# Kernel tuning notes

Hardware: AMD Instinct MI355X
Metric: run time of the kernel (lower is better)

## Reference

```python
import jax, jax.numpy as jnp
import numpy as np

SCALE = 16.0
IGNORE_THRESH = 0.5
BAD_CONF_WEIGHT = 1.25
NUM_CLASSES = 4
ANCHORS_PX = np.array([[16,16],[32,32],[64,64],[128,128],[256,256],[32,64],[64,32],[128,64],[64,128]], dtype=np.float32)


def _bce_logits(x, z):
    # stable binary_cross_entropy_with_logits, elementwise
    return jnp.maximum(x, 0.0) - x * z + jnp.log1p(jnp.exp(-jnp.abs(x)))


def _inv_tanh(y):
    mid = 0.5 * jnp.log((1.0 + y) / (1.0 - y))
    return jnp.where(y <= -1.0, -2.0, jnp.where(y >= 1.0, 2.0, mid))


def _iou_cxcywh(box1, box2):
    # matches bbox_iou(x1y1x2y2=False): (cx, cy, half_w, half_h) with +1 area convention
    b1x1, b1x2 = box1[:, 0] - box1[:, 2], box1[:, 0] + box1[:, 2]
    b1y1, b1y2 = box1[:, 1] - box1[:, 3], box1[:, 1] + box1[:, 3]
    b2x1, b2x2 = box2[:, 0] - box2[:, 2], box2[:, 0] + box2[:, 2]
    b2y1, b2y2 = box2[:, 1] - box2[:, 3], box2[:, 1] + box2[:, 3]
    iw = jnp.clip(jnp.minimum(b1x2, b2x2) - jnp.maximum(b1x1, b2x1) + 1.0, 0.0)
    ih = jnp.clip(jnp.minimum(b1y2, b2y2) - jnp.maximum(b1y1, b2y1) + 1.0, 0.0)
    inter = iw * ih
    a1 = (b1x2 - b1x1 + 1.0) * (b1y2 - b1y1 + 1.0)
    a2 = (b2x2 - b2x1 + 1.0) * (b2y2 - b2y1 + 1.0)
    return inter / (a1 + a2 - inter + 1e-16)


def _yolo_loss(prediction, target, target_sizes):
    nB, nA, nH, nW = prediction.shape[:4]
    nC = NUM_CLASSES
    anchors = jnp.asarray(ANCHORS_PX) / SCALE  # grid units, [nA,2]
    x = prediction[..., 1]
    y = prediction[..., 2]
    w = prediction[..., 5]
    h = prediction[..., 4]
    pred_conf = prediction[..., 0]
    pred_cls = prediction[..., 6:]
    grid_x = jnp.arange(nW, dtype=jnp.float32)[None, None, None, :]
    grid_y = jnp.arange(nH, dtype=jnp.float32)[None, None, :, None]
    aw4 = anchors[:, 0][None, :, None, None]
    ah4 = anchors[:, 1][None, :, None, None]
    xd, yd, wd, hd = map(jax.lax.stop_gradient, (x, y, w, h))  # torch uses .data
    pred_boxes = jnp.stack([
        jnp.tanh(xd) + 0.5 + grid_x + 0.0 * yd,
        jnp.tanh(yd) + 0.5 + grid_y + 0.0 * xd,
        jnp.exp(wd) * aw4,
        jnp.exp(hd) * ah4,
    ], axis=-1)  # [nB,nA,nH,nW,4]

    # target[:, :, [0,1,3,4]] /= scale (targets are constants w.r.t. grad)
    col_scale = jnp.ones(target.shape[-1], jnp.float32).at[jnp.array([0, 1, 3, 4])].set(1.0 / SCALE)
    tgt = jax.lax.stop_gradient(target) * col_scale

    pred_conf_sg = jax.lax.stop_gradient(pred_conf)
    pred_cls_sg = jax.lax.stop_gradient(pred_cls)
    b_idx = jnp.arange(nB)
    a_idx = jnp.arange(nA)
    awv = anchors[:, 0]
    ahv = anchors[:, 1]
    anchor_area = (awv + 1.0) * (ahv + 1.0)
    T = tgt.shape[1]
    ts_arr = target_sizes.astype(jnp.int32)
    zeros = jnp.zeros((nB, nA, nH, nW), jnp.float32)
    carry0 = dict(mask=zeros, conf_mask=jnp.ones_like(zeros), tx=zeros, ty=zeros, tw=zeros,
                  th=zeros, tconf=zeros, tcls=jnp.zeros((nB, nA, nH, nW, nC), jnp.float32),
                  nGT=jnp.zeros((), jnp.int32), nCorrect=jnp.zeros((), jnp.int32))

    def step(c, xs):
        t, row = xs  # row: [nB, 13+nC]
        gx, gy, gh_, gw_ = row[:, 0], row[:, 1], row[:, 3], row[:, 4]
        valid = (t < ts_arr) & (gw_ != 0) & (gh_ != 0)
        gi = jnp.clip(gx.astype(jnp.int32), 0, nW - 1)
        gj = jnp.clip(gy.astype(jnp.int32), 0, nH - 1)
        # anchor IoU (boxes [0,0,w,h] as corners, +1 convention) -> [nB,nA]
        inter = (jnp.minimum(gw_[:, None], awv[None, :]) + 1.0) * (jnp.minimum(gh_[:, None], ahv[None, :]) + 1.0)
        anch_ious = inter / ((gw_ + 1.0)[:, None] * (gh_ + 1.0)[:, None] + anchor_area[None, :] - inter + 1e-16)
        ii = (b_idx[:, None], a_idx[None, :], gj[:, None], gi[:, None])
        cm = c['conf_mask']
        cm = cm.at[ii].set(jnp.where(valid[:, None] & (anch_ious > IGNORE_THRESH), 0.0, cm[ii]))
        best_n = jnp.argmax(anch_ious, axis=1)
        idx = (b_idx, best_n, gj, gi)

        def setv(A, val):
            return A.at[idx].set(jnp.where(valid, val, A[idx]))

        mask = setv(c['mask'], 1.0)
        cm = setv(cm, 1.0)
        tx_ = setv(c['tx'], _inv_tanh(gx - (gi.astype(jnp.float32) + 0.5)))
        ty_ = setv(c['ty'], _inv_tanh(gy - (gj.astype(jnp.float32) + 0.5)))
        tw_ = setv(c['tw'], jnp.log(gw_ / awv[best_n] + 1e-16))
        th_ = setv(c['th'], jnp.log(gh_ / ahv[best_n] + 1e-16))
        tconf_ = setv(c['tconf'], 1.0)
        cls_row = row[:, 13:]
        tcls_ = c['tcls'].at[idx].set(jnp.where(valid[:, None], cls_row, c['tcls'][idx]))
        nGT = c['nGT'] + valid.sum().astype(jnp.int32)
        pb = pred_boxes[idx]  # [nB,4]
        iou = _iou_cxcywh(jnp.stack([gx, gy, gw_, gh_], axis=1), pb)
        plabel = jnp.argmax(pred_cls_sg[idx], axis=-1)
        score = pred_conf_sg[idx]
        correct = valid & (iou > 0.5) & (plabel == jnp.argmax(cls_row, axis=-1)) & (score > 0)
        nCorrect = c['nCorrect'] + correct.sum().astype(jnp.int32)
        return dict(mask=mask, conf_mask=cm, tx=tx_, ty=ty_, tw=tw_, th=th_, tconf=tconf_,
                    tcls=tcls_, nGT=nGT, nCorrect=nCorrect), None

    carry, _ = jax.lax.scan(step, carry0, (jnp.arange(T, dtype=jnp.int32), jnp.swapaxes(tgt, 0, 1)))

    mask = carry['mask']
    conf_mask = carry['conf_mask']
    cmf = conf_mask - mask  # conf_mask_false

    def masked_mean(v, m):
        return jnp.sum(v * m) / jnp.maximum(jnp.sum(m), 1.0)

    loss_conf = BAD_CONF_WEIGHT * masked_mean(_bce_logits(pred_conf, carry['tconf']), cmf)
    loss_x = masked_mean((x - carry['tx']) ** 2, mask)
    loss_y = masked_mean((y - carry['ty']) ** 2, mask)
    loss_w = masked_mean((w - carry['tw']) ** 2, mask)
    loss_h = masked_mean((h - carry['th']) ** 2, mask)
    labels = jnp.argmax(carry['tcls'], axis=-1)  # [nB,nA,nH,nW]
    ce = jax.nn.logsumexp(pred_cls, axis=-1) - jnp.take_along_axis(pred_cls, labels[..., None], axis=-1)[..., 0]
    loss_cls = masked_mean(ce, mask) / nB
    loss_conf = loss_conf + masked_mean(_bce_logits(pred_conf, carry['tconf']), mask)
    loss = loss_x + loss_y + loss_w + loss_h + loss_conf + loss_cls

    nGT = carry['nGT'].astype(jnp.float32)
    nCorrect = carry['nCorrect'].astype(jnp.float32)
    nProposals = jnp.sum(pred_conf_sg > 0).astype(jnp.float32)
    recall = jnp.where(nGT > 0, nCorrect / jnp.maximum(nGT, 1.0), 1.0)
    precision = jnp.where(nProposals > 0, nCorrect / jnp.maximum(nProposals, 1.0), 1.0)
    return loss, loss_x + loss_y + loss_w + loss_h, loss_conf, loss_cls, recall, precision


def setup_inputs() -> dict:
    key = jax.random.key(0)
    ks = jax.random.split(key, 7)
    nB, nA, nH, nW, nC, T = 16, 9, 128, 128, NUM_CLASSES, 50
    prediction = jax.random.normal(ks[0], (nB, nA, nH, nW, 6 + nC), dtype=jnp.float32)
    gx = jax.random.uniform(ks[1], (nB, T), dtype=jnp.float32) * (nW * SCALE)
    gy = jax.random.uniform(ks[2], (nB, T), dtype=jnp.float32) * (nH * SCALE)
    gh = jax.random.uniform(ks[3], (nB, T), dtype=jnp.float32) * 180.0 + 12.0
    gw = jax.random.uniform(ks[4], (nB, T), dtype=jnp.float32) * 180.0 + 12.0
    cls_idx = jax.random.randint(ks[5], (nB, T), 0, nC)
    target = jnp.zeros((nB, T, 13 + nC), jnp.float32)
    target = target.at[..., 0].set(gx).at[..., 1].set(gy).at[..., 3].set(gh).at[..., 4].set(gw)
    target = target.at[..., 13:].set(jax.nn.one_hot(cls_idx, nC, dtype=jnp.float32))
    target_sizes = jax.random.randint(ks[6], (nB,), 10, T + 1)
    return {"prediction": prediction, "target": target, "target_sizes": target_sizes}


def reference(prediction, target, target_sizes):
    return _yolo_loss(prediction, target, target_sizes)
```

## Files before the change

### kernel.cpp

```cpp
#include <hip/hip_runtime.h>
#include <math.h>

static constexpr int NA = 9;
static constexpr int NH = 128;
static constexpr int NW = 128;
static constexpr int NC = 4;
static constexpr int CH = 6 + NC;
static constexpr int TCOLS = 13 + NC;
static constexpr float SCALE_INV = 1.0f / 16.0f;
static constexpr int NBG = 2048;
static constexpr int SCAN_STRIDE = 16;
static constexpr int HSLOTS = 128;

__constant__ float c_aw[NA] = {1.f, 2.f, 4.f, 8.f, 16.f, 2.f, 4.f, 8.f, 4.f};
__constant__ float c_ah[NA] = {1.f, 2.f, 4.f, 8.f, 16.f, 4.f, 2.f, 4.f, 8.f};

static constexpr int NSLOT = 11;

__device__ __forceinline__ float bcef(float x, float z) {
    return fmaxf(x, 0.f) - x * z + log1pf(expf(-fabsf(x)));
}
__device__ __forceinline__ float invtanh(float y) {
    if (y <= -1.f) return -2.f;
    if (y >= 1.f) return 2.f;
    return 0.5f * logf((1.f + y) / (1.f - y));
}
__device__ __forceinline__ float wredf(float v) {
#pragma unroll
    for (int o = 32; o; o >>= 1) v += __shfl_down(v, o, 64);
    return v;
}

__global__ __launch_bounds__(256) void k_scan(const float* __restrict__ pred,
                                              const float* __restrict__ tgt,
                                              const int* __restrict__ tsz,
                                              float* __restrict__ scanPart, int T) {
    const int b = blockIdx.x;
    const int tid = threadIdx.x;
    const int lane = tid & 63;
    const int wave = tid >> 6;

    __shared__ int sPack[64], sTl[64], sSlot[64];
    __shared__ float sTx[64], sTy[64], sTw[64], sTh[64];
    __shared__ int sKey[HSLOTS];
    __shared__ int sPri[HSLOTS * NA];
    __shared__ int sBest[HSLOTS * NA];
    __shared__ float sAccW[4][NSLOT];

    for (int i = tid; i < HSLOTS; i += 256) sKey[i] = -1;
    for (int i = tid; i < HSLOTS * NA; i += 256) { sPri[i] = -1; sBest[i] = -1; }

    const int ts = tsz[b];
    float fGT = 0.f, fCor = 0.f;

    if (wave == 0 && lane < T) {
        const int t = lane;
        const float* row = tgt + (size_t)(b * T + t) * TCOLS;
        float gx = row[0] * SCALE_INV, gy = row[1] * SCALE_INV;
        float gh = row[3] * SCALE_INV, gw = row[4] * SCALE_INV;
        int valid = (t < ts) && (gw != 0.f) && (gh != 0.f);
        int gi = (int)gx; gi = gi < 0 ? 0 : (gi > NW - 1 ? NW - 1 : gi);
        int gj = (int)gy; gj = gj < 0 ? 0 : (gj > NH - 1 ? NH - 1 : gj);

        float bestIou = -1.f; int best = 0; int ign = 0;
#pragma unroll
        for (int a = 0; a < NA; a++) {
            float aw = c_aw[a], ah = c_ah[a];
            float inter = (fminf(gw, aw) + 1.f) * (fminf(gh, ah) + 1.f);
            float uni = (gw + 1.f) * (gh + 1.f) + (aw + 1.f) * (ah + 1.f) - inter + 1e-16f;
            float iou = inter / uni;
            if (iou > 0.5f) ign |= (1 << a);
            if (iou > bestIou) { bestIou = iou; best = a; }
        }
        sPack[t] = (valid ? 1 : 0) | (best << 1) | (ign << 5) | ((gj * NW + gi) << 14);
        sTx[t] = invtanh(gx - ((float)gi + 0.5f));
        sTy[t] = invtanh(gy - ((float)gj + 0.5f));
        sTw[t] = logf(gw / c_aw[best] + 1e-16f);
        sTh[t] = logf(gh / c_ah[best] + 1e-16f);

        float cc0 = row[13], cc1 = row[14], cc2 = row[15], cc3 = row[16];
        int tl = 0; float cmax = cc0;
        if (cc1 > cmax) { cmax = cc1; tl = 1; }
        if (cc2 > cmax) { cmax = cc2; tl = 2; }
        if (cc3 > cmax) { cmax = cc3; tl = 3; }
        sTl[t] = tl;

        if (valid) {
            fGT = 1.f;
            const float* p = pred + ((((size_t)b * NA + best) * NH + gj) * NW + gi) * CH;
            float p0 = p[0];
            float px = tanhf(p[1]) + 0.5f + (float)gi;
            float py = tanhf(p[2]) + 0.5f + (float)gj;
            float pw = expf(p[5]) * c_aw[best];
            float ph = expf(p[4]) * c_ah[best];
            float b1x1 = gx - gw, b1x2 = gx + gw, b1y1 = gy - gh, b1y2 = gy + gh;
            float b2x1 = px - pw, b2x2 = px + pw, b2y1 = py - ph, b2y2 = py + ph;
            float iw = fmaxf(fminf(b1x2, b2x2) - fmaxf(b1x1, b2x1) + 1.f, 0.f);
            float ih = fmaxf(fminf(b1y2, b2y2) - fmaxf(b1y1, b2y1) + 1.f, 0.f);
            float inter = iw * ih;
            float a1 = (b1x2 - b1x1 + 1.f) * (b1y2 - b1y1 + 1.f);
            float a2 = (b2x2 - b2x1 + 1.f) * (b2y2 - b2y1 + 1.f);
            float iou = inter / (a1 + a2 - inter + 1e-16f);
            float q0 = p[6], q1 = p[7], q2 = p[8], q3 = p[9];
            int pl = 0; float qm = q0;
            if (q1 > qm) { qm = q1; pl = 1; }
            if (q2 > qm) { qm = q2; pl = 2; }
            if (q3 > qm) { qm = q3; pl = 3; }
            if (iou > 0.5f && pl == tl && p0 > 0.f) fCor = 1.f;
        }
    }
    __syncthreads();

    if (tid < T) {
        int p = sPack[tid];
        if (p & 1) {
            int cell = p >> 14;
            int slot = cell & (HSLOTS - 1);
            while (true) {
                int old = atomicCAS(&sKey[slot], -1, cell);
                if (old == -1 || old == cell) break;
                slot = (slot + 1) & (HSLOTS - 1);
            }
            sSlot[tid] = slot;
        }
    }
    __syncthreads();

    for (int item = tid; item < T * NA; item += 256) {
        int t = item / NA, a = item - t * NA;
        int p = sPack[t];
        if (!(p & 1)) continue;
        int slot = sSlot[t];
        int best = (p >> 1) & 0xF;
        if (a == best) {
            atomicMax(&sPri[slot * NA + a], 2 * t + 1);
            atomicMax(&sBest[slot * NA + a], 2 * t + 1);
        } else if ((p >> (5 + a)) & 1) {
            atomicMax(&sPri[slot * NA + a], 2 * t);
        }
    }
    __syncthreads();

    float corrNum = 0.f, corrDen = 0.f, lconfM = 0.f, maskCnt = 0.f;
    float lx = 0.f, ly = 0.f, lw = 0.f, lh = 0.f, lcls = 0.f;
    for (int it = tid; it < HSLOTS * NA; it += 256) {
        int slot = it / NA, a = it - slot * NA;
        int cell = sKey[slot];
        if (cell < 0) continue;
        int pm = sPri[it];
        if (pm < 0) continue;
        int bm = sBest[it];
        const float* pp = pred + ((size_t)(b * NA + a) * (NH * NW) + cell) * CH;
        float conf = pp[0];
        float bce0 = bcef(conf, 0.f);
        if (bm >= 0) {
            float cm = (float)(pm & 1);
            float cmf = cm - 1.f;
            float bce1 = bcef(conf, 1.f);
            corrNum += bce1 * cmf - bce0;
            corrDen += cmf - 1.f;
            lconfM += bce1;
            maskCnt += 1.f;
            int t = bm >> 1;
            float dx = pp[1] - sTx[t], dy = pp[2] - sTy[t];
            float dw = pp[5] - sTw[t], dh = pp[4] - sTh[t];
            lx += dx * dx; ly += dy * dy; lw += dw * dw; lh += dh * dh;
            float q0 = pp[6], q1 = pp[7], q2 = pp[8], q3 = pp[9];
            float m = fmaxf(fmaxf(q0, q1), fmaxf(q2, q3));
            float lse = m + logf(expf(q0 - m) + expf(q1 - m) + expf(q2 - m) + expf(q3 - m));
            lcls += lse - pp[6 + sTl[t]];
        } else {
            corrNum -= bce0;
            corrDen -= 1.f;
        }
    }

    float v;
    v = wredf(corrNum); if (lane == 0) sAccW[wave][0] = v;
    v = wredf(corrDen); if (lane == 0) sAccW[wave][1] = v;
    v = wredf(maskCnt); if (lane == 0) sAccW[wave][2] = v;
    v = wredf(lx);      if (lane == 0) sAccW[wave][3] = v;
    v = wredf(ly);      if (lane == 0) sAccW[wave][4] = v;
    v = wredf(lw);      if (lane == 0) sAccW[wave][5] = v;
    v = wredf(lh);      if (lane == 0) sAccW[wave][6] = v;
    v = wredf(lcls);    if (lane == 0) sAccW[wave][7] = v;
    v = wredf(lconfM);  if (lane == 0) sAccW[wave][8] = v;
    v = wredf(fGT);     if (lane == 0) sAccW[wave][9] = v;
    v = wredf(fCor);    if (lane == 0) sAccW[wave][10] = v;
    __syncthreads();
    if (tid < NSLOT) {
        float s = sAccW[0][tid] + sAccW[1][tid] + sAccW[2][tid] + sAccW[3][tid];
        scanPart[b * SCAN_STRIDE + tid] = s;
    }
}

__global__ __launch_bounds__(256) void k_bg(const float* __restrict__ pred,
                                            float2* __restrict__ bgPart, int nCells) {
    __shared__ float sdat[2][4];
    float s0 = 0.f, npos = 0.f;
    const int stride = gridDim.x * blockDim.x;
#pragma unroll 4
    for (int c = blockIdx.x * blockDim.x + threadIdx.x; c < nCells; c += stride) {
        float cv = __builtin_nontemporal_load(&pred[(size_t)c * CH]);
        s0 += fmaxf(cv, 0.f) + log1pf(expf(-fabsf(cv)));
        npos += (cv > 0.f) ? 1.f : 0.f;
    }
    s0 = wredf(s0); npos = wredf(npos);
    int wid = threadIdx.x >> 6;
    if ((threadIdx.x & 63) == 0) { sdat[0][wid] = s0; sdat[1][wid] = npos; }
    __syncthreads();
    if (threadIdx.x == 0) {
        float a0 = sdat[0][0] + sdat[0][1] + sdat[0][2] + sdat[0][3];
        float a1 = sdat[1][0] + sdat[1][1] + sdat[1][2] + sdat[1][3];
        bgPart[blockIdx.x] = make_float2(a0, a1);
    }
}

__global__ __launch_bounds__(256) void k_fin(const float* __restrict__ scanPart,
                                             const float2* __restrict__ bgPart,
                                             float* __restrict__ out,
                                             double totalCells, int nB, int nbg) {
    __shared__ double sred[2][4];
    __shared__ double sscan[NSLOT];
    const int tid = threadIdx.x;

    double s0 = 0.0, np = 0.0;
    for (int i = tid; i < nbg; i += 256) {
        float2 v = bgPart[i];
        s0 += (double)v.x; np += (double)v.y;
    }
#pragma unroll
    for (int o = 32; o; o >>= 1) {
        s0 += __shfl_down(s0, o, 64);
        np += __shfl_down(np, o, 64);
    }
    int wid = tid >> 6;
    if ((tid & 63) == 0) { sred[0][wid] = s0; sred[1][wid] = np; }
    if (tid < NSLOT) {
        double s = 0.0;
        for (int b = 0; b < nB; b++) s += (double)scanPart[b * SCAN_STRIDE + tid];
        sscan[tid] = s;
    }
    __syncthreads();
    if (tid == 0) {
        double S0 = sred[0][0] + sred[0][1] + sred[0][2] + sred[0][3];
        double nProp = sred[1][0] + sred[1][1] + sred[1][2] + sred[1][3];
        double corrNum = sscan[0], corrDen = sscan[1], maskCnt = sscan[2];
        double lx = sscan[3], ly = sscan[4], lw = sscan[5], lh = sscan[6];
        double lcls = sscan[7], lconfM = sscan[8], nGT = sscan[9], nCor = sscan[10];

        double msum = fmax(maskCnt, 1.0);
        double cden = fmax(totalCells + corrDen, 1.0);
        double loss_conf = 1.25 * (S0 + corrNum) / cden + lconfM / msum;
        double lx_ = lx / msum, ly_ = ly / msum, lw_ = lw / msum, lh_ = lh / msum;
        double lcls_ = (lcls / msum) / (double)nB;
        double coord = lx_ + ly_ + lw_ + lh_;
        double loss = coord + loss_conf + lcls_;
        double recall = (nGT > 0.0) ? nCor / fmax(nGT, 1.0) : 1.0;
        double precision = (nProp > 0.0) ? nCor / fmax(nProp, 1.0) : 1.0;

        out[0] = (float)loss;
        out[1] = (float)coord;
        out[2] = (float)loss_conf;
        out[3] = (float)lcls_;
        out[4] = (float)recall;
        out[5] = (float)precision;
    }
}

extern "C" void kernel_launch(void* const* d_in, const int* in_sizes, int n_in,
                              void* d_out, int out_size, void* d_ws, size_t ws_size,
                              hipStream_t stream) {
    const float* pred = (const float*)d_in[0];
    const float* tgt = (const float*)d_in[1];
    const int* tsz = (const int*)d_in[2];
    int nB = in_sizes[2];
    int T = in_sizes[1] / (nB * TCOLS);
    long long total = (long long)nB * NA * NH * NW;
    int nCells = (int)total;

    float* scanPart = (float*)d_ws;
    float2* bgPart = (float2*)((char*)d_ws + (size_t)nB * SCAN_STRIDE * sizeof(float));
    float* out = (float*)d_out;

    hipLaunchKernelGGL(k_bg, dim3(NBG), dim3(256), 0, stream, pred, bgPart, nCells);
    hipLaunchKernelGGL(k_scan, dim3(nB), dim3(256), 0, stream, pred, tgt, tsz,
                       scanPart, T);
    hipLaunchKernelGGL(k_fin, dim3(1), dim3(256), 0, stream, scanPart, bgPart, out,
                       (double)total, nB, NBG);
}
```

Measured before the change: 37.76 us.

## Fuse scan, background and finalize kernels into one launch with last-block reduction

Merges the three kernels into a single kernel. The first nB blocks do the per-batch target scan, the remaining blocks do the background confidence reduction, and the last block to finish (found with an atomic counter and threadfence) does the final reduction. This removes two kernel launches and the gaps between them, at the cost of a memset before the launch and a larger shared-memory footprint per block, which could lower occupancy for the background blocks. The nontemporal load hint was also dropped.

```diff
diff --git a/kernel.cpp b/kernel.cpp
--- a/kernel.cpp
+++ b/kernel.cpp
@@ -30,241 +30,248 @@
     for (int o = 32; o; o >>= 1) v += __shfl_down(v, o, 64);
     return v;
 }
-
-__global__ __launch_bounds__(256) void k_scan(const float* __restrict__ pred,
-                                              const float* __restrict__ tgt,
-                                              const int* __restrict__ tsz,
-                                              float* __restrict__ scanPart, int T) {
-    const int b = blockIdx.x;
+__device__ __forceinline__ double wredd(double v) {
+#pragma unroll
+    for (int o = 32; o; o >>= 1) v += __shfl_down(v, o, 64);
+    return v;
+}
+
+__global__ __launch_bounds__(256) void k_all(
+    const float* __restrict__ pred, const float* __restrict__ tgt,
+    const int* __restrict__ tsz, float* __restrict__ scanPart,
+    float2* __restrict__ bgPart, unsigned int* __restrict__ doneCtr,
+    float* __restrict__ out, int nB, int T, int nCells, double totalCells) {
     const int tid = threadIdx.x;
     const int lane = tid & 63;
     const int wave = tid >> 6;
-
-    __shared__ int sPack[64], sTl[64], sSlot[64];
-    __shared__ float sTx[64], sTy[64], sTw[64], sTh[64];
-    __shared__ int sKey[HSLOTS];
-    __shared__ int sPri[HSLOTS * NA];
-    __shared__ int sBest[HSLOTS * NA];
-    __shared__ float sAccW[4][NSLOT];
-
-    for (int i = tid; i < HSLOTS; i += 256) sKey[i] = -1;
-    for (int i = tid; i < HSLOTS * NA; i += 256) { sPri[i] = -1; sBest[i] = -1; }
-
-    const int ts = tsz[b];
-    float fGT = 0.f, fCor = 0.f;
-
-    if (wave == 0 && lane < T) {
-        const int t = lane;
-        const float* row = tgt + (size_t)(b * T + t) * TCOLS;
-        float gx = row[0] * SCALE_INV, gy = row[1] * SCALE_INV;
-        float gh = row[3] * SCALE_INV, gw = row[4] * SCALE_INV;
-        int valid = (t < ts) && (gw != 0.f) && (gh != 0.f);
-        int gi = (int)gx; gi = gi < 0 ? 0 : (gi > NW - 1 ? NW - 1 : gi);
-        int gj = (int)gy; gj = gj < 0 ? 0 : (gj > NH - 1 ? NH - 1 : gj);
-
-        float bestIou = -1.f; int best = 0; int ign = 0;
+    const int nBlocksTotal = nB + NBG;
+
+    __shared__ int sFlag;
+
+    if ((int)blockIdx.x < nB) {
+        const int b = blockIdx.x;
+
+        __shared__ int sPack[64], sTl[64], sSlot[64];
+        __shared__ float sTx[64], sTy[64], sTw[64], sTh[64];
+        __shared__ int sKey[HSLOTS];
+        __shared__ int sPri[HSLOTS * NA];
+        __shared__ int sBest[HSLOTS * NA];
+        __shared__ float sAccW[4][NSLOT];
+
+        for (int i = tid; i < HSLOTS; i += 256) sKey[i] = -1;
+        for (int i = tid; i < HSLOTS * NA; i += 256) { sPri[i] = -1; sBest[i] = -1; }
+
+        const int ts = tsz[b];
+        float fGT = 0.f, fCor = 0.f;
+
+        if (wave == 0 && lane < T) {
+            const int t = lane;
+            const float* row = tgt + (size_t)(b * T + t) * TCOLS;
+            float gx = row[0] * SCALE_INV, gy = row[1] * SCALE_INV;
+            float gh = row[3] * SCALE_INV, gw = row[4] * SCALE_INV;
+            int valid = (t < ts) && (gw != 0.f) && (gh != 0.f);
+            int gi = (int)gx; gi = gi < 0 ? 0 : (gi > NW - 1 ? NW - 1 : gi);
+            int gj = (int)gy; gj = gj < 0 ? 0 : (gj > NH - 1 ? NH - 1 : gj);
+
+            float bestIou = -1.f; int best = 0; int ign = 0;
 #pragma unroll
-        for (int a = 0; a < NA; a++) {
-            float aw = c_aw[a], ah = c_ah[a];
-            float inter = (fminf(gw, aw) + 1.f) * (fminf(gh, ah) + 1.f);
-            float uni = (gw + 1.f) * (gh + 1.f) + (aw + 1.f) * (ah + 1.f) - inter + 1e-16f;
-            float iou = inter / uni;
-            if (iou > 0.5f) ign |= (1 << a);
-            if (iou > bestIou) { bestIou = iou; best = a; }
-        }
-        sPack[t] = (valid ? 1 : 0) | (best << 1) | (ign << 5) | ((gj * NW + gi) << 14);
-        sTx[t] = invtanh(gx - ((float)gi + 0.5f));
-        sTy[t] = invtanh(gy - ((float)gj + 0.5f));
-        sTw[t] = logf(gw / c_aw[best] + 1e-16f);
-        sTh[t] = logf(gh / c_ah[best] + 1e-16f);
-
-        float cc0 = row[13], cc1 = row[14], cc2 = row[15], cc3 = row[16];
-        int tl = 0; float cmax = cc0;
-        if (cc1 > cmax) { cmax = cc1; tl = 1; }
-        if (cc2 > cmax) { cmax = cc2; tl = 2; }
-        if (cc3 > cmax) { cmax = cc3; tl = 3; }
-        sTl[t] = tl;
-
-        if (valid) {
-            fGT = 1.f;
-            const float* p = pred + ((((size_t)b * NA + best) * NH + gj) * NW + gi) * CH;
-            float p0 = p[0];
-            float px = tanhf(p[1]) + 0.5f + (float)gi;
-            float py = tanhf(p[2]) + 0.5f + (float)gj;
-            float pw = expf(p[5]) * c_aw[best];
-            float ph = expf(p[4]) * c_ah[best];
-            float b1x1 = gx - gw, b1x2 = gx + gw, b1y1 = gy - gh, b1y2 = gy + gh;
-            float b2x1 = px - pw, b2x2 = px + pw, b2y1 = py - ph, b2y2 = py + ph;
-            float iw = fmaxf(fminf(b1x2, b2x2) - fmaxf(b1x1, b2x1) + 1.f, 0.f);
-            float ih = fmaxf(fminf(b1y2, b2y2) - fmaxf(b1y1, b2y1) + 1.f, 0.f);
-            float inter = iw * ih;
-            float a1 = (b1x2 - b1x1 + 1.f) * (b1y2 - b1y1 + 1.f);
-            float a2 = (b2x2 - b2x1 + 1.f) * (b2y2 - b2y1 + 1.f);
-            float iou = inter / (a1 + a2 - inter + 1e-16f);
-            float q0 = p[6], q1 = p[7], q2 = p[8], q3 = p[9];
-            int pl = 0; float qm = q0;
-            if (q1 > qm) { qm = q1; pl = 1; }
-            if (q2 > qm) { qm = q2; pl = 2; }
-            if (q3 > qm) { qm = q3; pl = 3; }
-            if (iou > 0.5f && pl == tl && p0 > 0.f) fCor = 1.f;
-        }
+            for (int a = 0; a < NA; a++) {
+                float aw = c_aw[a], ah = c_ah[a];
+                float inter = (fminf(gw, aw) + 1.f) * (fminf(gh, ah) + 1.f);
+                float uni = (gw + 1.f) * (gh + 1.f) + (aw + 1.f) * (ah + 1.f) - inter + 1e-16f;
+                float iou = inter / uni;
+                if (iou > 0.5f) ign |= (1 << a);
+                if (iou > bestIou) { bestIou = iou; best = a; }
+            }
+            sPack[t] = (valid ? 1 : 0) | (best << 1) | (ign << 5) | ((gj * NW + gi) << 14);
+            sTx[t] = invtanh(gx - ((float)gi + 0.5f));
+            sTy[t] = invtanh(gy - ((float)gj + 0.5f));
+            sTw[t] = logf(gw / c_aw[best] + 1e-16f);
+            sTh[t] = logf(gh / c_ah[best] + 1e-16f);
+
+            float cc0 = row[13], cc1 = row[14], cc2 = row[15], cc3 = row[16];
+            int tl = 0; float cmax = cc0;
+            if (cc1 > cmax) { cmax = cc1; tl = 1; }
+            if (cc2 > cmax) { cmax = cc2; tl = 2; }
+            if (cc3 > cmax) { cmax = cc3; tl = 3; }
+            sTl[t] = tl;
+
+            if (valid) {
+                fGT = 1.f;
+                const float* p = pred + ((((size_t)b * NA + best) * NH + gj) * NW + gi) * CH;
+                float p0 = p[0];
+                float px = tanhf(p[1]) + 0.5f + (float)gi;
+                float py = tanhf(p[2]) + 0.5f + (float)gj;
+                float pw = expf(p[5]) * c_aw[best];
+                float ph = expf(p[4]) * c_ah[best];
+                float b1x1 = gx - gw, b1x2 = gx + gw, b1y1 = gy - gh, b1y2 = gy + gh;
+                float b2x1 = px - pw, b2x2 = px + pw, b2y1 = py - ph, b2y2 = py + ph;
+                float iw = fmaxf(fminf(b1x2, b2x2) - fmaxf(b1x1, b2x1) + 1.f, 0.f);
+                float ih = fmaxf(fminf(b1y2, b2y2) - fmaxf(b1y1, b2y1) + 1.f, 0.f);
+                float inter = iw * ih;
+                float a1 = (b1x2 - b1x1 + 1.f) * (b1y2 - b1y1 + 1.f);
+                float a2 = (b2x2 - b2x1 + 1.f) * (b2y2 - b2y1 + 1.f);
+                float iou = inter / (a1 + a2 - inter + 1e-16f);
+                float q0 = p[6], q1 = p[7], q2 = p[8], q3 = p[9];
+                int pl = 0; float qm = q0;
+                if (q1 > qm) { qm = q1; pl = 1; }
+                if (q2 > qm) { qm = q2; pl = 2; }
+                if (q3 > qm) { qm = q3; pl = 3; }
+                if (iou > 0.5f && pl == tl && p0 > 0.f) fCor = 1.f;
+            }
+        }
+        __syncthreads();
+
+        if (tid < T) {
+            int p = sPack[tid];
+            if (p & 1) {
+                int cell = p >> 14;
+                int slot = cell & (HSLOTS - 1);
+                while (true) {
+                    int old = atomicCAS(&sKey[slot], -1, cell);
+                    if (old == -1 || old == cell) break;
+                    slot = (slot + 1) & (HSLOTS - 1);
+                }
+                sSlot[tid] = slot;
+            }
+        }
+        __syncthreads();
+
+        for (int item = tid; item < T * NA; item += 256) {
+            int t = item / NA, a = item - t * NA;
+            int p = sPack[t];
+            if (!(p & 1)) continue;
+            int slot = sSlot[t];
+            int best = (p >> 1) & 0xF;
+            if (a == best) {
+                atomicMax(&sPri[slot * NA + a], 2 * t + 1);
+                atomicMax(&sBest[slot * NA + a], 2 * t + 1);
+            } else if ((p >> (5 + a)) & 1) {
+                atomicMax(&sPri[slot * NA + a], 2 * t);
+            }
+        }
+        __syncthreads();
+
+        float corrNum = 0.f, corrDen = 0.f, lconfM = 0.f, maskCnt = 0.f;
+        float lx = 0.f, ly = 0.f, lw = 0.f, lh = 0.f, lcls = 0.f;
+        for (int it = tid; it < HSLOTS * NA; it += 256) {
+            int slot = it / NA, a = it - slot * NA;
+            int cell = sKey[slot];
+            if (cell < 0) continue;
+            int pm = sPri[it];
+            if (pm < 0) continue;
+            int bm = sBest[it];
+            const float* pp = pred + ((size_t)(b * NA + a) * (NH * NW) + cell) * CH;
+            float conf = pp[0];
+            float bce0 = bcef(conf, 0.f);
+            if (bm >= 0) {
+                float cm = (float)(pm & 1);
+                float cmf = cm - 1.f;
+                float bce1 = bcef(conf, 1.f);
+                corrNum += bce1 * cmf - bce0;
+                corrDen += cmf - 1.f;
+                lconfM += bce1;
+                maskCnt += 1.f;
+                int t = bm >> 1;
+                float dx = pp[1] - sTx[t], dy = pp[2] - sTy[t];
+                float dw = pp[5] - sTw[t], dh = pp[4] - sTh[t];
+                lx += dx * dx; ly += dy * dy; lw += dw * dw; lh += dh * dh;
+                float q0 = pp[6], q1 = pp[7], q2 = pp[8], q3 = pp[9];
+                float m = fmaxf(fmaxf(q0, q1), fmaxf(q2, q3));
+                float lse = m + logf(expf(q0 - m) + expf(q1 - m) + expf(q2 - m) + expf(q3 - m));
+                lcls += lse - pp[6 + sTl[t]];
+            } else {
+                corrNum -= bce0;
+                corrDen -= 1.f;
+            }
+        }
+
+        float v;
+        v = wredf(corrNum); if (lane == 0) sAccW[wave][0] = v;
+        v = wredf(corrDen); if (lane == 0) sAccW[wave][1] = v;
+        v = wredf(maskCnt); if (lane == 0) sAccW[wave][2] = v;
+        v = wredf(lx);      if (lane == 0) sAccW[wave][3] = v;
+        v = wredf(ly);      if (lane == 0) sAccW[wave][4] = v;
+        v = wredf(lw);      if (lane == 0) sAccW[wave][5] = v;
+        v = wredf(lh);      if (lane == 0) sAccW[wave][6] = v;
+        v = wredf(lcls);    if (lane == 0) sAccW[wave][7] = v;
+        v = wredf(lconfM);  if (lane == 0) sAccW[wave][8] = v;
+        v = wredf(fGT);     if (lane == 0) sAccW[wave][9] = v;
+        v = wredf(fCor);    if (lane == 0) sAccW[wave][10] = v;
+        __syncthreads();
+        if (tid < NSLOT) {
+            float s = sAccW[0][tid] + sAccW[1][tid] + sAccW[2][tid] + sAccW[3][tid];
+            scanPart[b * SCAN_STRIDE + tid] = s;
+        }
+    } else {
+        const int bgid = blockIdx.x - nB;
+        __shared__ float sdat[2][4];
+        float s0 = 0.f, npos = 0.f;
+        const int stride = NBG * 256;
+#pragma unroll 4
+        for (int c = bgid * 256 + tid; c < nCells; c += stride) {
+            float cv = pred[(size_t)c * CH];
+            s0 += fmaxf(cv, 0.f) + log1pf(expf(-fabsf(cv)));
+            npos += (cv > 0.f) ? 1.f : 0.f;
+        }
+        s0 = wredf(s0); npos = wredf(npos);
+        if (lane == 0) { sdat[0][wave] = s0; sdat[1][wave] = npos; }
+        __syncthreads();
+        if (tid == 0) {
+            float a0 = sdat[0][0] + sdat[0][1] + sdat[0][2] + sdat[0][3];
+            float a1 = sdat[1][0] + sdat[1][1] + sdat[1][2] + sdat[1][3];
+            bgPart[bgid] = make_float2(a0, a1);
+        }
+    }
+
+    __syncthreads();
+    if (tid == 0) {
+        __threadfence();
+        unsigned int old = atomicAdd(doneCtr, 1u);
+        sFlag = (old == (unsigned int)(nBlocksTotal - 1)) ? 1 : 0;
     }
     __syncthreads();
-
-    if (tid < T) {
-        int p = sPack[tid];
-        if (p & 1) {
-            int cell = p >> 14;
-            int slot = cell & (HSLOTS - 1);
-            while (true) {
-                int old = atomicCAS(&sKey[slot], -1, cell);
-                if (old == -1 || old == cell) break;
-                slot = (slot + 1) & (HSLOTS - 1);
-            }
-            sSlot[tid] = slot;
-        }
-    }
-    __syncthreads();
-
-    for (int item = tid; item < T * NA; item += 256) {
-        int t = item / NA, a = item - t * NA;
-        int p = sPack[t];
-        if (!(p & 1)) continue;
-        int slot = sSlot[t];
-        int best = (p >> 1) & 0xF;
-        if (a == best) {
-            atomicMax(&sPri[slot * NA + a], 2 * t + 1);
-            atomicMax(&sBest[slot * NA + a], 2 * t + 1);
-        } else if ((p >> (5 + a)) & 1) {
-            atomicMax(&sPri[slot * NA + a], 2 * t);
-        }
-    }
-    __syncthreads();
-
-    float corrNum = 0.f, corrDen = 0.f, lconfM = 0.f, maskCnt = 0.f;
-    float lx = 0.f, ly = 0.f, lw = 0.f, lh = 0.f, lcls = 0.f;
-    for (int it = tid; it < HSLOTS * NA; it += 256) {
-        int slot = it / NA, a = it - slot * NA;
-        int cell = sKey[slot];
-        if (cell < 0) continue;
-        int pm = sPri[it];
-        if (pm < 0) continue;
-        int bm = sBest[it];
-        const float* pp = pred + ((size_t)(b * NA + a) * (NH * NW) + cell) * CH;
-        float conf = pp[0];
-        float bce0 = bcef(conf, 0.f);
-        if (bm >= 0) {
-            float cm = (float)(pm & 1);
-            float cmf = cm - 1.f;
-            float bce1 = bcef(conf, 1.f);
-            corrNum += bce1 * cmf - bce0;
-            corrDen += cmf - 1.f;
-            lconfM += bce1;
-            maskCnt += 1.f;
-            int t = bm >> 1;
-            float dx = pp[1] - sTx[t], dy = pp[2] - sTy[t];
-            float dw = pp[5] - sTw[t], dh = pp[4] - sTh[t];
-            lx += dx * dx; ly += dy * dy; lw += dw * dw; lh += dh * dh;
-            float q0 = pp[6], q1 = pp[7], q2 = pp[8], q3 = pp[9];
-            float m = fmaxf(fmaxf(q0, q1), fmaxf(q2, q3));
-            float lse = m + logf(expf(q0 - m) + expf(q1 - m) + expf(q2 - m) + expf(q3 - m));
-            lcls += lse - pp[6 + sTl[t]];
-        } else {
-            corrNum -= bce0;
-            corrDen -= 1.f;
-        }
-    }
-
-    float v;
-    v = wredf(corrNum); if (lane == 0) sAccW[wave][0] = v;
-    v = wredf(corrDen); if (lane == 0) sAccW[wave][1] = v;
-    v = wredf(maskCnt); if (lane == 0) sAccW[wave][2] = v;
-    v = wredf(lx);      if (lane == 0) sAccW[wave][3] = v;
-    v = wredf(ly);      if (lane == 0) sAccW[wave][4] = v;
-    v = wredf(lw);      if (lane == 0) sAccW[wave][5] = v;
-    v = wredf(lh);      if (lane == 0) sAccW[wave][6] = v;
-    v = wredf(lcls);    if (lane == 0) sAccW[wave][7] = v;
-    v = wredf(lconfM);  if (lane == 0) sAccW[wave][8] = v;
-    v = wredf(fGT);     if (lane == 0) sAccW[wave][9] = v;
-    v = wredf(fCor);    if (lane == 0) sAccW[wave][10] = v;
-    __syncthreads();
-    if (tid < NSLOT) {
-        float s = sAccW[0][tid] + sAccW[1][tid] + sAccW[2][tid] + sAccW[3][tid];
-        scanPart[b * SCAN_STRIDE + tid] = s;
-    }
-}
-
-__global__ __launch_bounds__(256) void k_bg(const float* __restrict__ pred,
-                                            float2* __restrict__ bgPart, int nCells) {
-    __shared__ float sdat[2][4];
-    float s0 = 0.f, npos = 0.f;
-    const int stride = gridDim.x * blockDim.x;
-#pragma unroll 4
-    for (int c = blockIdx.x * blockDim.x + threadIdx.x; c < nCells; c += stride) {
-        float cv = __builtin_nontemporal_load(&pred[(size_t)c * CH]);
-        s0 += fmaxf(cv, 0.f) + log1pf(expf(-fabsf(cv)));
-        npos += (cv > 0.f) ? 1.f : 0.f;
-    }
-    s0 = wredf(s0); npos = wredf(npos);
-    int wid = threadIdx.x >> 6;
-    if ((threadIdx.x & 63) == 0) { sdat[0][wid] = s0; sdat[1][wid] = npos; }
-    __syncthreads();
-    if (threadIdx.x == 0) {
-        float a0 = sdat[0][0] + sdat[0][1] + sdat[0][2] + sdat[0][3];
-        float a1 = sdat[1][0] + sdat[1][1] + sdat[1][2] + sdat[1][3];
-        bgPart[blockIdx.x] = make_float2(a0, a1);
-    }
-}
-
-__global__ __launch_bounds__(256) void k_fin(const float* __restrict__ scanPart,
-                                             const float2* __restrict__ bgPart,
-                                             float* __restrict__ out,
-                                             double totalCells, int nB, int nbg) {
-    __shared__ double sred[2][4];
-    __shared__ double sscan[NSLOT];
-    const int tid = threadIdx.x;
-
-    double s0 = 0.0, np = 0.0;
-    for (int i = tid; i < nbg; i += 256) {
-        float2 v = bgPart[i];
-        s0 += (double)v.x; np += (double)v.y;
-    }
-#pragma unroll
-    for (int o = 32; o; o >>= 1) {
-        s0 += __shfl_down(s0, o, 64);
-        np += __shfl_down(np, o, 64);
-    }
-    int wid = tid >> 6;
-    if ((tid & 63) == 0) { sred[0][wid] = s0; sred[1][wid] = np; }
-    if (tid < NSLOT) {
-        double s = 0.0;
-        for (int b = 0; b < nB; b++) s += (double)scanPart[b * SCAN_STRIDE + tid];
-        sscan[tid] = s;
-    }
-    __syncthreads();
-    if (tid == 0) {
-        double S0 = sred[0][0] + sred[0][1] + sred[0][2] + sred[0][3];
-        double nProp = sred[1][0] + sred[1][1] + sred[1][2] + sred[1][3];
-        double corrNum = sscan[0], corrDen = sscan[1], maskCnt = sscan[2];
-        double lx = sscan[3], ly = sscan[4], lw = sscan[5], lh = sscan[6];
-        double lcls = sscan[7], lconfM = sscan[8], nGT = sscan[9], nCor = sscan[10];
-
-        double msum = fmax(maskCnt, 1.0);
-        double cden = fmax(totalCells + corrDen, 1.0);
-        double loss_conf = 1.25 * (S0 + corrNum) / cden + lconfM / msum;
-        double lx_ = lx / msum, ly_ = ly / msum, lw_ = lw / msum, lh_ = lh / msum;
-        double lcls_ = (lcls / msum) / (double)nB;
-        double coord = lx_ + ly_ + lw_ + lh_;
-        double loss = coord + loss_conf + lcls_;
-        double recall = (nGT > 0.0) ? nCor / fmax(nGT, 1.0) : 1.0;
-        double precision = (nProp > 0.0) ? nCor / fmax(nProp, 1.0) : 1.0;
-
-        out[0] = (float)loss;
-        out[1] = (float)coord;
-        out[2] = (float)loss_conf;
-        out[3] = (float)lcls_;
-        out[4] = (float)recall;
-        out[5] = (float)precision;
+    if (sFlag) {
+        __threadfence();
+        __shared__ double dR[2][4];
+        __shared__ double dScan[NSLOT];
+        double s0 = 0.0, np = 0.0;
+        for (int i = tid; i < NBG; i += 256) {
+            float2 v = bgPart[i];
+            s0 += (double)v.x; np += (double)v.y;
+        }
+        s0 = wredd(s0); np = wredd(np);
+        if (lane == 0) { dR[0][wave] = s0; dR[1][wave] = np; }
+        if (tid < NSLOT) {
+            double s = 0.0;
+            for (int b2 = 0; b2 < nB; b2++) s += (double)scanPart[b2 * SCAN_STRIDE + tid];
+            dScan[tid] = s;
+        }
+        __syncthreads();
+        if (tid == 0) {
+            double S0 = dR[0][0] + dR[0][1] + dR[0][2] + dR[0][3];
+            double nProp = dR[1][0] + dR[1][1] + dR[1][2] + dR[1][3];
+            double corrNum = dScan[0], corrDen = dScan[1], maskCnt = dScan[2];
+            double lx = dScan[3], ly = dScan[4], lw = dScan[5], lh = dScan[6];
+            double lcls = dScan[7], lconfM = dScan[8], nGT = dScan[9], nCor = dScan[10];
+
+            double msum = fmax(maskCnt, 1.0);
+            double cden = fmax(totalCells + corrDen, 1.0);
+            double loss_conf = 1.25 * (S0 + corrNum) / cden + lconfM / msum;
+            double lx_ = lx / msum, ly_ = ly / msum, lw_ = lw / msum, lh_ = lh / msum;
+            double lcls_ = (lcls / msum) / (double)nB;
+            double coord = lx_ + ly_ + lw_ + lh_;
+            double loss = coord + loss_conf + lcls_;
+            double recall = (nGT > 0.0) ? nCor / fmax(nGT, 1.0) : 1.0;
+            double precision = (nProp > 0.0) ? nCor / fmax(nProp, 1.0) : 1.0;
+
+            out[0] = (float)loss;
+            out[1] = (float)coord;
+            out[2] = (float)loss_conf;
+            out[3] = (float)lcls_;
+            out[4] = (float)recall;
+            out[5] = (float)precision;
+        }
     }
 }
 
@@ -281,11 +288,11 @@
 
     float* scanPart = (float*)d_ws;
     float2* bgPart = (float2*)((char*)d_ws + (size_t)nB * SCAN_STRIDE * sizeof(float));
+    unsigned int* doneCtr =
+        (unsigned int*)((char*)bgPart + (size_t)NBG * sizeof(float2));
     float* out = (float*)d_out;
 
-    hipLaunchKernelGGL(k_bg, dim3(NBG), dim3(256), 0, stream, pred, bgPart, nCells);
-    hipLaunchKernelGGL(k_scan, dim3(nB), dim3(256), 0, stream, pred, tgt, tsz,
-                       scanPart, T);
-    hipLaunchKernelGGL(k_fin, dim3(1), dim3(256), 0, stream, scanPart, bgPart, out,
-                       (double)total, nB, NBG);
-}
+    hipMemsetAsync(doneCtr, 0, sizeof(unsigned int), stream);
+    hipLaunchKernelGGL(k_all, dim3(nB + NBG), dim3(256), 0, stream, pred, tgt, tsz,
+                       scanPart, bgPart, doneCtr, out, nB, T, nCells, (double)total);
+}
```

After: 92.79 us. +145.7%, slower.
